# Optimization experiments

Hardware: AMD Instinct MI355X
Metric: run time of the kernel (lower is better)

The kernel has to match this reference:

```python
import jax, jax.numpy as jnp
import numpy as np


def _sage_conv(x, src, dst, W_l, b_l, W_r, num_nodes):
    # PyG SAGEConv (aggr='mean'): out = lin_l(mean_j x[src_j]) + lin_r(x)
    msg = x[src]                                                  # [E, d]
    agg = jax.ops.segment_sum(msg, dst, num_segments=num_nodes)   # [N, d]
    deg = jax.ops.segment_sum(jnp.ones_like(dst, dtype=x.dtype), dst,
                              num_segments=num_nodes)             # [N]
    mean = agg / jnp.maximum(deg, 1.0)[:, None]
    return mean @ W_l + b_l + x @ W_r


def setup_inputs() -> dict:
    key = jax.random.key(0)
    ks = jax.random.split(key, 8)
    N, E, D = 50000, 640000, 128
    s = 1.0 / np.sqrt(D)
    return {
        "x": jax.random.normal(ks[0], (N, D), dtype=jnp.float32),
        "edge_index": jax.random.randint(ks[1], (2, E), 0, N, dtype=jnp.int64),
        "W1_l": jax.random.normal(ks[2], (D, D), dtype=jnp.float32) * s,
        "b1_l": jnp.zeros((D,), dtype=jnp.float32),
        "W1_r": jax.random.normal(ks[3], (D, D), dtype=jnp.float32) * s,
        "W2_l": jax.random.normal(ks[4], (D, D), dtype=jnp.float32) * s,
        "b2_l": jnp.zeros((D,), dtype=jnp.float32),
        "W2_r": jax.random.normal(ks[5], (D, D), dtype=jnp.float32) * s,
    }


def reference(x, edge_index, W1_l, b1_l, W1_r, W2_l, b2_l, W2_r):
    N = x.shape[0]
    src, dst = edge_index[0], edge_index[1]
    h = jax.nn.relu(_sage_conv(x, src, dst, W1_l, b1_l, W1_r, N))
    z = _sage_conv(h, src, dst, W2_l, b2_l, W2_r, N)
    return z
```

## Files before the change

### kernel.cpp

```cpp
#include <hip/hip_runtime.h>
#include <hip/hip_bf16.h>


#define CAP 64

typedef __attribute__((ext_vector_type(8))) short short8v;
typedef __attribute__((ext_vector_type(4))) float float4v;

__device__ __forceinline__ ushort f2bf(float f) {
    unsigned u = __float_as_uint(f);
    u += 0x7fff + ((u >> 16) & 1);
    return (ushort)(u >> 16);
}

#if __has_builtin(__builtin_amdgcn_cvt_pk_fp8_f32) && __has_builtin(__builtin_amdgcn_cvt_f32_fp8)
#define HW_FP8 1
#endif

__device__ __forceinline__ float fp8_dec_sw(unsigned b) {
    unsigned s = b >> 7, e = (b >> 3) & 15, m = b & 7;
    float v = e ? __uint_as_float(((e + 120u) << 23) | (m << 20))
                : (float)m * 0.001953125f;
    return s ? -v : v;
}
__device__ __forceinline__ unsigned fp8_enc_sw(float f) {
    float aa = fabsf(f);
    unsigned e32 = __float_as_uint(aa) >> 23;
    float c = (aa < 0.015625f) ? 16384.f : __uint_as_float((e32 + 20) << 23);
    float r = (aa + c) - c;
    if (r > 448.f) r = 448.f;
    unsigned s = (__float_as_uint(f) >> 31) << 7;
    if (r == 0.f) return s;
    unsigned u = __float_as_uint(r);
    int e = (int)(u >> 23) - 127;
    if (e < -6) return s | (unsigned)(r * 512.f);
    return s | ((unsigned)(e + 7) << 3) | ((u >> 20) & 7);
}

__device__ __forceinline__ unsigned enc4_fp8(float4 v) {
#ifdef HW_FP8
    int p = 0;
    p = __builtin_amdgcn_cvt_pk_fp8_f32(v.x, v.y, p, false);
    p = __builtin_amdgcn_cvt_pk_fp8_f32(v.z, v.w, p, true);
    return (unsigned)p;
#else
    return fp8_enc_sw(v.x) | (fp8_enc_sw(v.y) << 8) |
           (fp8_enc_sw(v.z) << 16) | (fp8_enc_sw(v.w) << 24);
#endif
}
__device__ __forceinline__ unsigned char enc1_fp8(float v) {
#ifdef HW_FP8
    return (unsigned char)(__builtin_amdgcn_cvt_pk_fp8_f32(v, v, 0, false) & 0xff);
#else
    return (unsigned char)fp8_enc_sw(v);
#endif
}
template <int SEL>
__device__ __forceinline__ float dec_fp8(unsigned w) {
#ifdef HW_FP8
    return __builtin_amdgcn_cvt_f32_fp8(w, SEL);
#else
    return fp8_dec_sw((w >> (SEL * 8)) & 0xff);
#endif
}
__device__ __forceinline__ void acc4_fp8(float* a, unsigned w) {
    a[0] += dec_fp8<0>(w);
    a[1] += dec_fp8<1>(w);
    a[2] += dec_fp8<2>(w);
    a[3] += dec_fp8<3>(w);
}

__global__ __launch_bounds__(256) void prep_a_kernel(
    const float* __restrict__ X, ushort* __restrict__ Xb,
    unsigned* __restrict__ X8, int n4,
    const float* __restrict__ W1l, const float* __restrict__ W1r, ushort* __restrict__ Wt1,
    const float* __restrict__ W2l, const float* __restrict__ W2r, ushort* __restrict__ Wt2,
    uint4* __restrict__ cursor4, int nCur4,
    int nConv) {
    int b = blockIdx.x;
    if (b < nConv) {
        int i = b * 256 + threadIdx.x;
        if (i < n4) {
            float4 v = reinterpret_cast<const float4*>(X)[i];
            ushort4 o;
            o.x = f2bf(v.x); o.y = f2bf(v.y); o.z = f2bf(v.z); o.w = f2bf(v.w);
            reinterpret_cast<ushort4*>(Xb)[i] = o;
            X8[i] = enc4_fp8(v);
        }
    } else if (b < nConv + 256) {
        int wb = b - nConv;
        const float* Wl = (wb < 128) ? W1l : W2l;
        const float* Wr = (wb < 128) ? W1r : W2r;
        ushort* Wt = (wb < 128) ? Wt1 : Wt2;
        int col = wb & 127;
        int k = threadIdx.x;
        float v = (k < 128) ? Wl[k * 128 + col] : Wr[(k - 128) * 128 + col];
        Wt[col * 256 + k] = f2bf(v);
    } else {
        int i = (b - nConv - 256) * 256 + threadIdx.x;
        if (i < nCur4) cursor4[i] = make_uint4(0, 0, 0, 0);
    }
}

__global__ __launch_bounds__(256) void fill_kernel(
    const int* __restrict__ src, const int* __restrict__ dst, int E, int N,
    int* __restrict__ cursor, ushort* __restrict__ csrc) {
    const int slice = blockIdx.x & 7;
    const int chunk = blockIdx.x >> 3;
    int e = chunk * 256 + threadIdx.x;
    if (e < E) {
        int d = dst[e];
        const int lo = (slice * N) >> 3;
        const int hi = ((slice + 1) * N) >> 3;
        if (d >= lo && d < hi) {
            int pos = atomicAdd(&cursor[d], 1);
            if (pos < CAP) csrc[(size_t)d * CAP + pos] = (ushort)src[e];
        }
    }
}

__global__ __launch_bounds__(256) void gather_mean_fp8(
    const unsigned* __restrict__ X8, const int* __restrict__ cnt,
    const ushort* __restrict__ csrc, ushort* __restrict__ meanb, int N) {
    const int wid = (blockIdx.x * 256 + threadIdx.x) >> 6;
    if (wid >= N) return;
    const int lane = threadIdx.x & 63;
    const int q = lane >> 4;
    const int lq = lane & 15;
    const int dc = min(cnt[wid], CAP);
    const ushort* ep = csrc + (size_t)wid * CAP;

    float acc[8];
#pragma unroll
    for (int j = 0; j < 8; ++j) acc[j] = 0.f;

    const uint2* Xp = reinterpret_cast<const uint2*>(X8);
    int e = 0;
#pragma unroll 2
    for (; e + 3 < dc; e += 4) {
        int s = ep[e + q];
        uint2 v = Xp[(size_t)s * 16 + lq];
        acc4_fp8(acc, v.x);
        acc4_fp8(acc + 4, v.y);
    }
    if (e + q < dc) {
        int s = ep[e + q];
        uint2 v = Xp[(size_t)s * 16 + lq];
        acc4_fp8(acc, v.x);
        acc4_fp8(acc + 4, v.y);
    }

#pragma unroll
    for (int j = 0; j < 8; ++j) {
        acc[j] += __shfl_xor(acc[j], 32);
        acc[j] += __shfl_xor(acc[j], 16);
    }

    if (q == 0) {
        float sc = 1.0f / (float)max(dc, 1);
        uint4 o;
        o.x = (unsigned)f2bf(acc[0] * sc) | ((unsigned)f2bf(acc[1] * sc) << 16);
        o.y = (unsigned)f2bf(acc[2] * sc) | ((unsigned)f2bf(acc[3] * sc) << 16);
        o.z = (unsigned)f2bf(acc[4] * sc) | ((unsigned)f2bf(acc[5] * sc) << 16);
        o.w = (unsigned)f2bf(acc[6] * sc) | ((unsigned)f2bf(acc[7] * sc) << 16);
        reinterpret_cast<uint4*>(meanb)[(size_t)wid * 16 + lq] = o;
    }
}


template <int RELU, int OUT_BF16, int WRITE_FP8>
__global__ __launch_bounds__(256) void sage_gemm_mfma(
    const ushort* __restrict__ A0,
    const ushort* __restrict__ A1,
    const ushort* __restrict__ Wt,
    const float* __restrict__ bias,
    void* __restrict__ outv,
    unsigned char* __restrict__ out8, int N) {
    __shared__ __align__(16) ushort Ws[128 * 256];
    const int tid = threadIdx.x;
    const int lane = tid & 63;
    const int wave = tid >> 6;
    const int r = lane & 15;
    const int g = lane >> 4;
    const int row0 = blockIdx.x * 64 + wave * 16;

    int ar = row0 + r;
    if (ar >= N) ar = N - 1;

    const ushort* Arow0 = A0 + (size_t)ar * 128;
    const ushort* Arow1 = A1 + (size_t)ar * 128;

    short8v af[8];
#pragma unroll
    for (int ks = 0; ks < 8; ++ks) {
        const ushort* Ap = (ks < 4) ? Arow0 : Arow1;
        af[ks] = *(const short8v*)(Ap + (ks & 3) * 32 + g * 8);
    }

    {
        const uint4* Wg = reinterpret_cast<const uint4*>(Wt);
        uint4* Ls = reinterpret_cast<uint4*>(Ws);
#pragma unroll
        for (int it = 0; it < 16; ++it) {
            int G = it * 256 + tid;
            int col = G >> 5, gr = G & 31;
            Ls[col * 32 + (gr ^ (col & 7))] = Wg[G];
        }
    }

    float4v acc[8];
#pragma unroll
    for (int ct = 0; ct < 8; ++ct) {
        float bv = bias[ct * 16 + r];
        acc[ct] = (float4v){bv, bv, bv, bv};
    }

    __syncthreads();

#pragma unroll
    for (int ks = 0; ks < 8; ++ks) {
#pragma unroll
        for (int ct = 0; ct < 8; ++ct) {
            const int col = ct * 16 + r;
            const int gr = (ks * 4 + g) ^ (r & 7);
            short8v bf = *(const short8v*)(Ws + col * 256 + gr * 8);
            acc[ct] = __builtin_amdgcn_mfma_f32_16x16x32_bf16(af[ks], bf, acc[ct], 0, 0, 0);
        }
    }

#pragma unroll
    for (int ct = 0; ct < 8; ++ct) {
        const int col = ct * 16 + r;
#pragma unroll
        for (int reg = 0; reg < 4; ++reg) {
            int orow = row0 + g * 4 + reg;
            if (orow < N) {
                float v = acc[ct][reg];
                if (RELU) v = fmaxf(v, 0.f);
                if (OUT_BF16)
                    ((ushort*)outv)[(size_t)orow * 128 + col] = f2bf(v);
                else
                    ((float*)outv)[(size_t)orow * 128 + col] = v;
                if (WRITE_FP8)
                    out8[(size_t)orow * 128 + col] = enc1_fp8(v);
            }
        }
    }
}


extern "C" void kernel_launch(void* const* d_in, const int* in_sizes, int n_in,
                              void* d_out, int out_size, void* d_ws, size_t ws_size,
                              hipStream_t stream) {
    const float* x   = (const float*)d_in[0];
    const int*   ei  = (const int*)d_in[1];
    const float* W1l = (const float*)d_in[2];
    const float* b1  = (const float*)d_in[3];
    const float* W1r = (const float*)d_in[4];
    const float* W2l = (const float*)d_in[5];
    const float* b2  = (const float*)d_in[6];
    const float* W2r = (const float*)d_in[7];
    float* out = (float*)d_out;

    const int D = 128;
    const int N = in_sizes[0] / D;
    const int E = in_sizes[1] / 2;

    const int* srcp = ei;
    const int* dstp = ei + E;

    char* ws = (char*)d_ws;
    ushort*   xb     = (ushort*)ws;
    ushort*   hb     = xb + (size_t)N * D;
    ushort*   meanb  = hb + (size_t)N * D;
    ushort*   Wt1    = meanb + (size_t)N * D;
    ushort*   Wt2    = Wt1 + 128 * 256;
    unsigned* x8     = (unsigned*)(Wt2 + 128 * 256);
    unsigned* h8     = x8 + (size_t)N * D / 4;
    ushort*   csrc   = (ushort*)(h8 + (size_t)N * D / 4);
    int*      cursor = (int*)(csrc + (size_t)N * CAP);

    const int n4 = N * D / 4;
    const int nConv = (n4 + 255) / 256;
    const int nCur4 = (N + 3) / 4;
    const int nZero = (nCur4 + 255) / 256;

    prep_a_kernel<<<nConv + 256 + nZero, 256, 0, stream>>>(
        x, xb, x8, n4, W1l, W1r, Wt1, W2l, W2r, Wt2,
        (uint4*)cursor, nCur4, nConv);

    const int nChunk = (E + 255) / 256;
    fill_kernel<<<8 * nChunk, 256, 0, stream>>>(srcp, dstp, E, N, cursor, csrc);

    const int gather_blocks = (N * 64 + 255) / 256;
    const int gemm_blocks = (N + 63) / 64;

    gather_mean_fp8<<<gather_blocks, 256, 0, stream>>>(x8, cursor, csrc, meanb, N);
    sage_gemm_mfma<1, 1, 1><<<gemm_blocks, 256, 0, stream>>>(
        meanb, xb, Wt1, b1, hb, (unsigned char*)h8, N);

    gather_mean_fp8<<<gather_blocks, 256, 0, stream>>>(h8, cursor, csrc, meanb, N);
    sage_gemm_mfma<0, 0, 0><<<gemm_blocks, 256, 0, stream>>>(
        meanb, hb, Wt2, b2, out, nullptr, N);
}
```

Baseline: 118.7 us.

## Fuse CSR fill into prep kernel, vectorize edge loads, double GEMM row tile

```diff
diff --git a/kernel.cpp b/kernel.cpp
--- a/kernel.cpp
+++ b/kernel.cpp
@@ -70,16 +70,45 @@
     a[3] += dec_fp8<3>(w);
 }
 
-__global__ __launch_bounds__(256) void prep_a_kernel(
+__global__ __launch_bounds__(256) void zero_kernel(uint4* __restrict__ c4, int n) {
+    int i = blockIdx.x * 256 + threadIdx.x;
+    if (i < n) c4[i] = make_uint4(0, 0, 0, 0);
+}
+
+#define NFILL 2048
+__global__ __launch_bounds__(256) void prep_fill_kernel(
+    const int* __restrict__ src, const int* __restrict__ dst, int E, int N,
+    int* __restrict__ cursor, ushort* __restrict__ csrc,
     const float* __restrict__ X, ushort* __restrict__ Xb,
     unsigned* __restrict__ X8, int n4,
     const float* __restrict__ W1l, const float* __restrict__ W1r, ushort* __restrict__ Wt1,
     const float* __restrict__ W2l, const float* __restrict__ W2r, ushort* __restrict__ Wt2,
-    uint4* __restrict__ cursor4, int nCur4,
     int nConv) {
     int b = blockIdx.x;
-    if (b < nConv) {
-        int i = b * 256 + threadIdx.x;
+    if (b < NFILL) {
+        const int slice = b & 7;
+        const int lo = (slice * N) >> 3;
+        const int hi = ((slice + 1) * N) >> 3;
+        const int nChunk4 = (E / 4 + 255) / 256;
+        const int4* d4p = reinterpret_cast<const int4*>(dst);
+        const int4* s4p = reinterpret_cast<const int4*>(src);
+        for (int chunk = b >> 3; chunk < nChunk4; chunk += NFILL / 8) {
+            int e4 = chunk * 256 + threadIdx.x;
+            if (e4 * 4 < E) {
+                int4 d4 = d4p[e4];
+                int4 s4 = s4p[e4];
+#pragma unroll
+                for (int j = 0; j < 4; ++j) {
+                    int d = (&d4.x)[j];
+                    if (d >= lo && d < hi) {
+                        int pos = atomicAdd(&cursor[d], 1);
+                        if (pos < CAP) csrc[(size_t)d * CAP + pos] = (ushort)(&s4.x)[j];
+                    }
+                }
+            }
+        }
+    } else if (b < NFILL + nConv) {
+        int i = (b - NFILL) * 256 + threadIdx.x;
         if (i < n4) {
             float4 v = reinterpret_cast<const float4*>(X)[i];
             ushort4 o;
@@ -87,8 +116,8 @@
             reinterpret_cast<ushort4*>(Xb)[i] = o;
             X8[i] = enc4_fp8(v);
         }
-    } else if (b < nConv + 256) {
-        int wb = b - nConv;
+    } else {
+        int wb = b - NFILL - nConv;
         const float* Wl = (wb < 128) ? W1l : W2l;
         const float* Wr = (wb < 128) ? W1r : W2r;
         ushort* Wt = (wb < 128) ? Wt1 : Wt2;
@@ -96,33 +125,14 @@
         int k = threadIdx.x;
         float v = (k < 128) ? Wl[k * 128 + col] : Wr[(k - 128) * 128 + col];
         Wt[col * 256 + k] = f2bf(v);
-    } else {
-        int i = (b - nConv - 256) * 256 + threadIdx.x;
-        if (i < nCur4) cursor4[i] = make_uint4(0, 0, 0, 0);
-    }
-}
-
-__global__ __launch_bounds__(256) void fill_kernel(
-    const int* __restrict__ src, const int* __restrict__ dst, int E, int N,
-    int* __restrict__ cursor, ushort* __restrict__ csrc) {
-    const int slice = blockIdx.x & 7;
-    const int chunk = blockIdx.x >> 3;
-    int e = chunk * 256 + threadIdx.x;
-    if (e < E) {
-        int d = dst[e];
-        const int lo = (slice * N) >> 3;
-        const int hi = ((slice + 1) * N) >> 3;
-        if (d >= lo && d < hi) {
-            int pos = atomicAdd(&cursor[d], 1);
-            if (pos < CAP) csrc[(size_t)d * CAP + pos] = (ushort)src[e];
-        }
-    }
-}
+    }
+}
+
 
 __global__ __launch_bounds__(256) void gather_mean_fp8(
     const unsigned* __restrict__ X8, const int* __restrict__ cnt,
     const ushort* __restrict__ csrc, ushort* __restrict__ meanb, int N) {
-    const int wid = (blockIdx.x * 256 + threadIdx.x) >> 6;
+    const int wid = __builtin_amdgcn_readfirstlane((blockIdx.x * 256 + threadIdx.x) >> 6);
     if (wid >= N) return;
     const int lane = threadIdx.x & 63;
     const int q = lane >> 4;
@@ -138,7 +148,9 @@
     int e = 0;
 #pragma unroll 2
     for (; e + 3 < dc; e += 4) {
-        int s = ep[e + q];
+        uint2 iw = *reinterpret_cast<const uint2*>(ep + e);
+        unsigned wv = (q & 2) ? iw.y : iw.x;
+        int s = (q & 1) ? (int)(wv >> 16) : (int)(wv & 0xffff);
         uint2 v = Xp[(size_t)s * 16 + lq];
         acc4_fp8(acc, v.x);
         acc4_fp8(acc + 4, v.y);
@@ -182,19 +194,18 @@
     const int wave = tid >> 6;
     const int r = lane & 15;
     const int g = lane >> 4;
-    const int row0 = blockIdx.x * 64 + wave * 16;
-
-    int ar = row0 + r;
-    if (ar >= N) ar = N - 1;
-
-    const ushort* Arow0 = A0 + (size_t)ar * 128;
-    const ushort* Arow1 = A1 + (size_t)ar * 128;
-
-    short8v af[8];
+    const int rt0 = blockIdx.x * 128 + wave * 32;
+
+    int ar0 = rt0 + r;       if (ar0 >= N) ar0 = N - 1;
+    int ar1 = rt0 + 16 + r;  if (ar1 >= N) ar1 = N - 1;
+
+    short8v af0[8], af1[8];
 #pragma unroll
     for (int ks = 0; ks < 8; ++ks) {
-        const ushort* Ap = (ks < 4) ? Arow0 : Arow1;
-        af[ks] = *(const short8v*)(Ap + (ks & 3) * 32 + g * 8);
+        const ushort* Ap0 = ((ks < 4) ? A0 : A1) + (size_t)ar0 * 128;
+        const ushort* Ap1 = ((ks < 4) ? A0 : A1) + (size_t)ar1 * 128;
+        af0[ks] = *(const short8v*)(Ap0 + (ks & 3) * 32 + g * 8);
+        af1[ks] = *(const short8v*)(Ap1 + (ks & 3) * 32 + g * 8);
     }
 
     {
@@ -208,11 +219,12 @@
         }
     }
 
-    float4v acc[8];
+    float4v acc0[8], acc1[8];
 #pragma unroll
     for (int ct = 0; ct < 8; ++ct) {
         float bv = bias[ct * 16 + r];
-        acc[ct] = (float4v){bv, bv, bv, bv};
+        acc0[ct] = (float4v){bv, bv, bv, bv};
+        acc1[ct] = acc0[ct];
     }
 
     __syncthreads();
@@ -224,25 +236,31 @@
             const int col = ct * 16 + r;
             const int gr = (ks * 4 + g) ^ (r & 7);
             short8v bf = *(const short8v*)(Ws + col * 256 + gr * 8);
-            acc[ct] = __builtin_amdgcn_mfma_f32_16x16x32_bf16(af[ks], bf, acc[ct], 0, 0, 0);
-        }
-    }
-
-#pragma unroll
-    for (int ct = 0; ct < 8; ++ct) {
-        const int col = ct * 16 + r;
-#pragma unroll
-        for (int reg = 0; reg < 4; ++reg) {
-            int orow = row0 + g * 4 + reg;
-            if (orow < N) {
-                float v = acc[ct][reg];
-                if (RELU) v = fmaxf(v, 0.f);
-                if (OUT_BF16)
-                    ((ushort*)outv)[(size_t)orow * 128 + col] = f2bf(v);
-                else
-                    ((float*)outv)[(size_t)orow * 128 + col] = v;
-                if (WRITE_FP8)
-                    out8[(size_t)orow * 128 + col] = enc1_fp8(v);
+            acc0[ct] = __builtin_amdgcn_mfma_f32_16x16x32_bf16(af0[ks], bf, acc0[ct], 0, 0, 0);
+            acc1[ct] = __builtin_amdgcn_mfma_f32_16x16x32_bf16(af1[ks], bf, acc1[ct], 0, 0, 0);
+        }
+    }
+
+#pragma unroll
+    for (int t = 0; t < 2; ++t) {
+        const int rbase = rt0 + t * 16;
+        float4v* acc = t ? acc1 : acc0;
+#pragma unroll
+        for (int ct = 0; ct < 8; ++ct) {
+            const int col = ct * 16 + r;
+#pragma unroll
+            for (int reg = 0; reg < 4; ++reg) {
+                int orow = rbase + g * 4 + reg;
+                if (orow < N) {
+                    float v = acc[ct][reg];
+                    if (RELU) v = fmaxf(v, 0.f);
+                    if (OUT_BF16)
+                        ((ushort*)outv)[(size_t)orow * 128 + col] = f2bf(v);
+                    else
+                        ((float*)outv)[(size_t)orow * 128 + col] = v;
+                    if (WRITE_FP8)
+                        out8[(size_t)orow * 128 + col] = enc1_fp8(v);
+                }
             }
         }
     }
@@ -283,17 +301,15 @@
     const int n4 = N * D / 4;
     const int nConv = (n4 + 255) / 256;
     const int nCur4 = (N + 3) / 4;
-    const int nZero = (nCur4 + 255) / 256;
-
-    prep_a_kernel<<<nConv + 256 + nZero, 256, 0, stream>>>(
-        x, xb, x8, n4, W1l, W1r, Wt1, W2l, W2r, Wt2,
-        (uint4*)cursor, nCur4, nConv);
-
-    const int nChunk = (E + 255) / 256;
-    fill_kernel<<<8 * nChunk, 256, 0, stream>>>(srcp, dstp, E, N, cursor, csrc);
+
+    zero_kernel<<<(nCur4 + 255) / 256, 256, 0, stream>>>((uint4*)cursor, nCur4);
+
+    prep_fill_kernel<<<NFILL + nConv + 256, 256, 0, stream>>>(
+        srcp, dstp, E, N, cursor, csrc, x, xb, x8, n4,
+        W1l, W1r, Wt1, W2l, W2r, Wt2, nConv);
 
     const int gather_blocks = (N * 64 + 255) / 256;
-    const int gemm_blocks = (N + 63) / 64;
+    const int gemm_blocks = (N + 127) / 128;
 
     gather_mean_fp8<<<gather_blocks, 256, 0, stream>>>(x8, cursor, csrc, meanb, N);
     sage_gemm_mfma<1, 1, 1><<<gemm_blocks, 256, 0, stream>>>(
```

Measured after the change: 115.1 us. 1.03x faster.
